# Kernel optimization log

Hardware: AMD Instinct MI355X
Metric: run time of the kernel (lower is better)

The kernel has to match this reference:

```python
import jax, jax.numpy as jnp
import numpy as np

D_EMBED = 1024


def setup_inputs() -> dict:
    key = jax.random.key(0)
    ks = jax.random.split(key, 8)
    B, S, D = 8, 2048, D_EMBED
    scale = 1.0 / np.sqrt(D)
    return {
        "embeddings": jax.random.normal(ks[0], (B, S, D), dtype=jnp.float32),
        "mask": jnp.zeros((B, S, S), dtype=jnp.float32),
        "Wq": jax.random.normal(ks[1], (D, D), dtype=jnp.float32) * scale,
        "bq": jax.random.normal(ks[2], (D,), dtype=jnp.float32) * 0.02,
        "Wk": jax.random.normal(ks[3], (D, D), dtype=jnp.float32) * scale,
        "bk": jax.random.normal(ks[4], (D,), dtype=jnp.float32) * 0.02,
        "Wv": jax.random.normal(ks[5], (D, D), dtype=jnp.float32) * scale,
        "bv": jax.random.normal(ks[6], (D,), dtype=jnp.float32) * 0.02,
    }


def reference(embeddings, mask, Wq, bq, Wk, bk, Wv, bv):
    # torch Linear: y = x @ W.T + b
    q = jnp.einsum('bsd,ed->bse', embeddings, Wq) + bq
    k = jnp.einsum('bsd,ed->bse', embeddings, Wk) + bk
    v = jnp.einsum('bsd,ed->bse', embeddings, Wv) + bv
    scores = jnp.einsum('bqd,bkd->bqk', q, k)
    # NOTE: faithful to source — mask added BEFORE scaling by 1/sqrt(d)
    scores = (scores + mask) * (1.0 / jnp.sqrt(jnp.float32(q.shape[-1])))
    attn = jax.nn.softmax(scores, axis=-1)
    return jnp.einsum('bqk,bkd->bqd', attn, v)
```

## Files before the change

### kernel.cpp

```cpp
#include <hip/hip_runtime.h>


#define B_SZ 8
#define SEQ  2048
#define DIM  1024
#define MROWS (B_SZ * SEQ)

typedef unsigned short u16;
typedef short short8 __attribute__((ext_vector_type(8)));
typedef unsigned short u16x4 __attribute__((ext_vector_type(4)));
typedef float f32x4 __attribute__((ext_vector_type(4)));

__device__ __forceinline__ u16 f2bf(float x) {
  unsigned int u = __float_as_uint(x);
  return (u16)((u + 0x7fffu + ((u >> 16) & 1u)) >> 16);
}
__device__ __forceinline__ float bf2f(u16 h) {
  return __uint_as_float(((unsigned int)h) << 16);
}

__device__ __forceinline__ int xcd_swz(int x, int nwg) {
  return (x & 7) * (nwg >> 3) + (x >> 3);
}

__device__ __forceinline__ void gload_lds16(const u16* g, u16* l) {
  __builtin_amdgcn_global_load_lds(
      (__attribute__((address_space(1))) void*)(g),
      (__attribute__((address_space(3))) void*)(l), 16, 0, 0);
}

__device__ __forceinline__ f32x4 mfma_bf16(short8 a, short8 b, f32x4 c) {
  asm("v_mfma_f32_16x16x32_bf16 %0, %1, %2, %0" : "+v"(c) : "v"(a), "v"(b));
  return c;
}

__device__ __forceinline__ void gemm256_core(const u16* __restrict__ Ag,
                                             const u16* __restrict__ Bg,
                                             int NT, size_t lda, size_t ldb,
                                             u16* sm, f32x4 (&acc)[8][4]) {
  const int tid = threadIdx.x;
  const int lane = tid & 63;
  const int wid = tid >> 6;
  const int wm = wid >> 2;
  const int wn = wid & 3;
  const int wm8 = wm << 3;
  const int wn4 = wn << 2;

  u16* sA = sm;
  u16* sB = sm + 32768;

  const int bb = (lane << 4) ^ (((lane >> 5) & 1) << 5);
  const int rins = bb >> 6;
  const int cins = (bb & 63) >> 1;
  const int s0 = wid, s1 = 8 + wid, s2 = 16 + wid, s3 = 24 + wid;
  const size_t aoff0 = (size_t)((s0 >> 1) * 16 + rins) * lda + ((s0 & 1) * 32 + cins);
  const size_t aoff1 = (size_t)((s1 >> 1) * 16 + rins) * lda + ((s1 & 1) * 32 + cins);
  const size_t aoff2 = (size_t)((s2 >> 1) * 16 + rins) * lda + ((s2 & 1) * 32 + cins);
  const size_t aoff3 = (size_t)((s3 >> 1) * 16 + rins) * lda + ((s3 & 1) * 32 + cins);
  const size_t boff0 = (size_t)((s0 >> 1) * 16 + rins) * ldb + ((s0 & 1) * 32 + cins);
  const size_t boff1 = (size_t)((s1 >> 1) * 16 + rins) * ldb + ((s1 & 1) * 32 + cins);
  const size_t boff2 = (size_t)((s2 >> 1) * 16 + rins) * ldb + ((s2 & 1) * 32 + cins);
  const size_t boff3 = (size_t)((s3 >> 1) * 16 + rins) * ldb + ((s3 & 1) * 32 + cins);
  const int wid512 = wid << 9;

  const int lof = ((lane & 15) << 6) + ((lane >> 4) << 4);
  const int loe = (lof ^ (((lane >> 3) & 1) << 5)) >> 1;

#define ISSUE_A(j, nb, kt) \
  gload_lds16(Ag + aoff##j + (size_t)(kt) * 64, sA + (nb) * 16384 + (j) * 4096 + wid512)
#define ISSUE_B(j, nb, kt) \
  gload_lds16(Bg + boff##j + (size_t)(kt) * 64, sB + (nb) * 16384 + (j) * 4096 + wid512)

  ISSUE_B(0, 0, 0); ISSUE_B(1, 0, 0); ISSUE_B(2, 0, 0); ISSUE_B(3, 0, 0);
  ISSUE_A(0, 0, 0); ISSUE_A(1, 0, 0); ISSUE_A(2, 0, 0); ISSUE_A(3, 0, 0);

  int buf = 0;
  for (int kt = 0; kt < NT; ++kt) {
    const int nk = kt + 1;
    const bool pre = nk < NT;
    const int nb = buf ^ 1;
    asm volatile("s_waitcnt vmcnt(1)" ::: "memory");
    __builtin_amdgcn_s_barrier();
    asm volatile("" ::: "memory");
    const u16* bufA = sA + buf * 16384;
    const u16* bufB = sB + buf * 16384;
    short8 bf[4][2];
#pragma unroll
    for (int n = 0; n < 4; ++n) {
      bf[n][0] = *(const short8*)(bufB + (wn4 + n) * 1024 + loe);
      bf[n][1] = *(const short8*)(bufB + (wn4 + n) * 1024 + 512 + loe);
    }
    {
      short8 af[2][2];
#pragma unroll
      for (int m = 0; m < 2; ++m) {
        af[m][0] = *(const short8*)(bufA + (wm8 + m) * 1024 + loe);
        af[m][1] = *(const short8*)(bufA + (wm8 + m) * 1024 + 512 + loe);
      }
      if (pre) { ISSUE_B(0, nb, nk); ISSUE_B(1, nb, nk); }
      __builtin_amdgcn_s_setprio(1);
#pragma unroll
      for (int m = 0; m < 2; ++m)
#pragma unroll
        for (int n = 0; n < 4; ++n) {
          acc[m][n] = mfma_bf16(af[m][0], bf[n][0], acc[m][n]);
          acc[m][n] = mfma_bf16(af[m][1], bf[n][1], acc[m][n]);
        }
      __builtin_amdgcn_s_setprio(0);
    }
    {
      short8 af[2][2];
#pragma unroll
      for (int m = 0; m < 2; ++m) {
        af[m][0] = *(const short8*)(bufA + (wm8 + 2 + m) * 1024 + loe);
        af[m][1] = *(const short8*)(bufA + (wm8 + 2 + m) * 1024 + 512 + loe);
      }
      if (pre) { ISSUE_B(2, nb, nk); ISSUE_B(3, nb, nk); }
      __builtin_amdgcn_s_setprio(1);
#pragma unroll
      for (int m = 0; m < 2; ++m)
#pragma unroll
        for (int n = 0; n < 4; ++n) {
          acc[2 + m][n] = mfma_bf16(af[m][0], bf[n][0], acc[2 + m][n]);
          acc[2 + m][n] = mfma_bf16(af[m][1], bf[n][1], acc[2 + m][n]);
        }
      __builtin_amdgcn_s_setprio(0);
    }
    if (pre) {
      asm volatile("s_waitcnt vmcnt(4)" ::: "memory");
    } else {
      asm volatile("s_waitcnt vmcnt(0)" ::: "memory");
    }
    __builtin_amdgcn_s_barrier();
    asm volatile("" ::: "memory");
    {
      short8 af[2][2];
#pragma unroll
      for (int m = 0; m < 2; ++m) {
        af[m][0] = *(const short8*)(bufA + (wm8 + 4 + m) * 1024 + loe);
        af[m][1] = *(const short8*)(bufA + (wm8 + 4 + m) * 1024 + 512 + loe);
      }
      if (pre) { ISSUE_A(0, nb, nk); ISSUE_A(1, nb, nk); }
      __builtin_amdgcn_s_setprio(1);
#pragma unroll
      for (int m = 0; m < 2; ++m)
#pragma unroll
        for (int n = 0; n < 4; ++n) {
          acc[4 + m][n] = mfma_bf16(af[m][0], bf[n][0], acc[4 + m][n]);
          acc[4 + m][n] = mfma_bf16(af[m][1], bf[n][1], acc[4 + m][n]);
        }
      __builtin_amdgcn_s_setprio(0);
    }
    {
      short8 af[2][2];
#pragma unroll
      for (int m = 0; m < 2; ++m) {
        af[m][0] = *(const short8*)(bufA + (wm8 + 6 + m) * 1024 + loe);
        af[m][1] = *(const short8*)(bufA + (wm8 + 6 + m) * 1024 + 512 + loe);
      }
      if (pre) { ISSUE_A(2, nb, nk); ISSUE_A(3, nb, nk); }
      __builtin_amdgcn_s_setprio(1);
#pragma unroll
      for (int m = 0; m < 2; ++m)
#pragma unroll
        for (int n = 0; n < 4; ++n) {
          acc[6 + m][n] = mfma_bf16(af[m][0], bf[n][0], acc[6 + m][n]);
          acc[6 + m][n] = mfma_bf16(af[m][1], bf[n][1], acc[6 + m][n]);
        }
      __builtin_amdgcn_s_setprio(0);
    }
    buf ^= 1;
  }
  asm volatile("s_nop 7\n\ts_nop 7\n\ts_nop 7" ::);
#undef ISSUE_A
#undef ISSUE_B
}

__global__ __launch_bounds__(256) void cvt_kernel(const float* __restrict__ in,
                                                  u16* __restrict__ out, int n4) {
  int i = blockIdx.x * 256 + threadIdx.x;
  if (i >= n4) return;
  float4 v = ((const float4*)in)[i];
  u16x4 o;
  o[0] = f2bf(v.x); o[1] = f2bf(v.y); o[2] = f2bf(v.z); o[3] = f2bf(v.w);
  ((u16x4*)out)[i] = o;
}

__global__ __launch_bounds__(512) void proj256_kernel(const u16* __restrict__ emb16,
                                                      const u16* __restrict__ Bq,
                                                      const u16* __restrict__ Bk,
                                                      const u16* __restrict__ Bv,
                                                      const float* __restrict__ bq,
                                                      const float* __restrict__ bk,
                                                      const float* __restrict__ bv,
                                                      u16* __restrict__ q16,
                                                      u16* __restrict__ k16,
                                                      u16* __restrict__ vT) {
  __shared__ __align__(16) u16 sm[65536];
  const int wg = xcd_swz(blockIdx.x, 768);
  const int lane = threadIdx.x & 63, wid = threadIdx.x >> 6;
  f32x4 acc[8][4] = {};
  if (wg < 512) {
    const int m0 = (wg >> 3) * 256;
    const int z = (wg >> 2) & 1;
    const int n0 = (wg & 3) * 256;
    gemm256_core(emb16 + (size_t)m0 * 1024, (z ? Bk : Bq) + (size_t)n0 * 1024,
                 16, 1024, 1024, sm, acc);
    const int rb = m0 + ((wid >> 2) << 7) + ((lane >> 4) << 2);
    const int cb = n0 + ((wid & 3) << 6) + (lane & 15);
    const float* bias = z ? bk : bq;
    u16* dst = z ? k16 : q16;
#pragma unroll
    for (int m = 0; m < 8; ++m)
#pragma unroll
      for (int n = 0; n < 4; ++n)
#pragma unroll
        for (int j = 0; j < 4; ++j) {
          int row = rb + m * 16 + j;
          int col = cb + n * 16;
          dst[(size_t)row * DIM + col] = f2bf(acc[m][n][j] + bias[col]);
        }
  } else {
    const int r = wg - 512;
    const int m0 = (r & 3) * 256;
    const int n0 = (r >> 2) * 256;
    gemm256_core(Bv + (size_t)m0 * 1024, emb16 + (size_t)n0 * 1024,
                 16, 1024, 1024, sm, acc);
    const int rb = m0 + ((wid >> 2) << 7) + ((lane >> 4) << 2);
    const int cb = n0 + ((wid & 3) << 6) + (lane & 15);
#pragma unroll
    for (int m = 0; m < 8; ++m)
#pragma unroll
      for (int n = 0; n < 4; ++n)
#pragma unroll
        for (int j = 0; j < 4; ++j) {
          int d = rb + m * 16 + j;
          int kg = cb + n * 16;
          int bi = kg >> 11, s = kg & 2047;
          vT[((size_t)bi << 21) + ((size_t)d << 11) + s] = f2bf(acc[m][n][j] + bv[d]);
        }
  }
}

__global__ __launch_bounds__(512) void scores256_kernel(const u16* __restrict__ q16,
                                                        const u16* __restrict__ k16,
                                                        const float* __restrict__ mask,
                                                        float* __restrict__ scF) {
  __shared__ __align__(16) u16 sm[65536];
  const int wg = xcd_swz(blockIdx.x, 512);
  const int b = wg >> 6;
  const int m0 = ((wg >> 3) & 7) * 256;
  const int n0 = (wg & 7) * 256;
  f32x4 acc[8][4] = {};
  gemm256_core(q16 + ((size_t)b * SEQ + m0) * DIM, k16 + ((size_t)b * SEQ + n0) * DIM,
               16, DIM, DIM, sm, acc);
  const int lane = threadIdx.x & 63, wid = threadIdx.x >> 6;
  const int rb = m0 + ((wid >> 2) << 7) + ((lane >> 4) << 2);
  const int cb = n0 + ((wid & 3) << 6) + (lane & 15);
#pragma unroll
  for (int m = 0; m < 8; ++m)
#pragma unroll
    for (int n = 0; n < 4; ++n)
#pragma unroll
      for (int j = 0; j < 4; ++j) {
        size_t idx = ((size_t)b * SEQ + rb + m * 16 + j) * SEQ + (cb + n * 16);
        scF[idx] = (acc[m][n][j] + mask[idx]) * 0.03125f;
      }
}

__global__ __launch_bounds__(512) void pv256_kernel(const u16* __restrict__ pr,
                                                    const u16* __restrict__ vt,
                                                    float* __restrict__ out) {
  __shared__ __align__(16) u16 sm[65536];
  const int wg = xcd_swz(blockIdx.x, 256);
  const int b = wg >> 5;
  const int m0 = ((wg >> 2) & 7) * 256;
  const int n0 = (wg & 3) * 256;
  f32x4 acc[8][4] = {};
  gemm256_core(pr + ((size_t)b * SEQ + m0) * (2 * SEQ), vt + ((size_t)b * DIM + n0) * SEQ,
               32, 2 * SEQ, SEQ, sm, acc);
  const int lane = threadIdx.x & 63, wid = threadIdx.x >> 6;
  const int rb = m0 + ((wid >> 2) << 7) + ((lane >> 4) << 2);
  const int cb = n0 + ((wid & 3) << 6) + (lane & 15);
#pragma unroll
  for (int m = 0; m < 8; ++m)
#pragma unroll
    for (int n = 0; n < 4; ++n)
#pragma unroll
      for (int j = 0; j < 4; ++j)
        out[((size_t)b * SEQ + rb + m * 16 + j) * DIM + (cb + n * 16)] = acc[m][n][j];
}

__global__ __launch_bounds__(256) void softmax_kernel(float* __restrict__ scF) {
  __shared__ float red[8];
  const size_t row = blockIdx.x;
  float* rowp = scF + row * SEQ;
  const int tid = threadIdx.x;
  float4 v0 = ((const float4*)rowp)[2 * tid];
  float4 v1 = ((const float4*)rowp)[2 * tid + 1];
  float f[8] = {v0.x, v0.y, v0.z, v0.w, v1.x, v1.y, v1.z, v1.w};
  float mx = f[0];
#pragma unroll
  for (int j = 1; j < 8; ++j) mx = fmaxf(mx, f[j]);
#pragma unroll
  for (int off = 1; off < 64; off <<= 1) mx = fmaxf(mx, __shfl_xor(mx, off));
  const int wid = tid >> 6, lane = tid & 63;
  if (lane == 0) red[wid] = mx;
  __syncthreads();
  mx = fmaxf(fmaxf(red[0], red[1]), fmaxf(red[2], red[3]));
  float e[8];
  float s = 0.f;
#pragma unroll
  for (int j = 0; j < 8; ++j) {
    e[j] = __expf(f[j] - mx);
    s += e[j];
  }
#pragma unroll
  for (int off = 1; off < 64; off <<= 1) s += __shfl_xor(s, off);
  if (lane == 0) red[4 + wid] = s;
  __syncthreads();
  s = (red[4] + red[5]) + (red[6] + red[7]);
  const float inv = 1.f / s;
  short8 o;
#pragma unroll
  for (int j = 0; j < 8; ++j) o[j] = (short)f2bf(e[j] * inv);
  *(short8*)((u16*)rowp + tid * 8) = o;
}

extern "C" void kernel_launch(void* const* d_in, const int* in_sizes, int n_in,
                              void* d_out, int out_size, void* d_ws, size_t ws_size,
                              hipStream_t stream) {
  const float* emb  = (const float*)d_in[0];
  const float* mask = (const float*)d_in[1];
  const float* Wq   = (const float*)d_in[2];
  const float* bq   = (const float*)d_in[3];
  const float* Wk   = (const float*)d_in[4];
  const float* bk   = (const float*)d_in[5];
  const float* Wv   = (const float*)d_in[6];
  const float* bv   = (const float*)d_in[7];
  float* out = (float*)d_out;

  const size_t M1 = 1024 * 1024;
  float* scF  = (float*)d_ws;
  u16* emb16 = (u16*)d_ws + 64 * M1;
  u16* Bq  = emb16 + 16 * M1;
  u16* Bk  = Bq + 1 * M1;
  u16* Bv  = Bk + 1 * M1;
  u16* q16 = Bv + 1 * M1;
  u16* k16 = q16 + 16 * M1;
  u16* vT  = k16 + 16 * M1;

  cvt_kernel<<<16384, 256, 0, stream>>>(emb, emb16, (int)(4 * M1));
  cvt_kernel<<<1024, 256, 0, stream>>>(Wq, Bq, (int)(M1 / 4));
  cvt_kernel<<<1024, 256, 0, stream>>>(Wk, Bk, (int)(M1 / 4));
  cvt_kernel<<<1024, 256, 0, stream>>>(Wv, Bv, (int)(M1 / 4));

  proj256_kernel<<<768, 512, 0, stream>>>(emb16, Bq, Bk, Bv, bq, bk, bv, q16, k16, vT);

  scores256_kernel<<<512, 512, 0, stream>>>(q16, k16, mask, scF);
  softmax_kernel<<<MROWS, 256, 0, stream>>>(scF);
  pv256_kernel<<<256, 512, 0, stream>>>((const u16*)scF, vT, out);
}
```

Measured before the change: 326.0 us.

## Switch to fp16 MFMA and store scores as fp16, moving mask add to softmax

All GEMM operands and intermediates go from bf16 to fp16 with v_mfma_f32_16x16x32_f16. The score matrix is now written as fp16 instead of fp32, which halves the traffic of writing, reading and rewriting the 8x2048x2048 scores. The mask read moves from the scores epilogue into the softmax kernel. fp16 has a narrower range than bf16, so there is some overflow risk, and scores are rounded to fp16 before softmax.

```diff
diff --git a/kernel.cpp b/kernel.cpp
--- a/kernel.cpp
+++ b/kernel.cpp
@@ -11,12 +11,12 @@
 typedef unsigned short u16x4 __attribute__((ext_vector_type(4)));
 typedef float f32x4 __attribute__((ext_vector_type(4)));
 
-__device__ __forceinline__ u16 f2bf(float x) {
-  unsigned int u = __float_as_uint(x);
-  return (u16)((u + 0x7fffu + ((u >> 16) & 1u)) >> 16);
-}
-__device__ __forceinline__ float bf2f(u16 h) {
-  return __uint_as_float(((unsigned int)h) << 16);
+__device__ __forceinline__ u16 f2h(float x) {
+  _Float16 h = (_Float16)x;
+  union { _Float16 f; u16 u; } c; c.f = h; return c.u;
+}
+__device__ __forceinline__ float h2f(u16 u) {
+  union { _Float16 f; u16 u; } c; c.u = u; return (float)c.f;
 }
 
 __device__ __forceinline__ int xcd_swz(int x, int nwg) {
@@ -29,8 +29,8 @@
       (__attribute__((address_space(3))) void*)(l), 16, 0, 0);
 }
 
-__device__ __forceinline__ f32x4 mfma_bf16(short8 a, short8 b, f32x4 c) {
-  asm("v_mfma_f32_16x16x32_bf16 %0, %1, %2, %0" : "+v"(c) : "v"(a), "v"(b));
+__device__ __forceinline__ f32x4 mfma_f16(short8 a, short8 b, f32x4 c) {
+  asm("v_mfma_f32_16x16x32_f16 %0, %1, %2, %0" : "+v"(c) : "v"(a), "v"(b));
   return c;
 }
 
@@ -103,8 +103,8 @@
       for (int m = 0; m < 2; ++m)
 #pragma unroll
         for (int n = 0; n < 4; ++n) {
-          acc[m][n] = mfma_bf16(af[m][0], bf[n][0], acc[m][n]);
-          acc[m][n] = mfma_bf16(af[m][1], bf[n][1], acc[m][n]);
+          acc[m][n] = mfma_f16(af[m][0], bf[n][0], acc[m][n]);
+          acc[m][n] = mfma_f16(af[m][1], bf[n][1], acc[m][n]);
         }
       __builtin_amdgcn_s_setprio(0);
     }
@@ -121,8 +121,8 @@
       for (int m = 0; m < 2; ++m)
 #pragma unroll
         for (int n = 0; n < 4; ++n) {
-          acc[2 + m][n] = mfma_bf16(af[m][0], bf[n][0], acc[2 + m][n]);
-          acc[2 + m][n] = mfma_bf16(af[m][1], bf[n][1], acc[2 + m][n]);
+          acc[2 + m][n] = mfma_f16(af[m][0], bf[n][0], acc[2 + m][n]);
+          acc[2 + m][n] = mfma_f16(af[m][1], bf[n][1], acc[2 + m][n]);
         }
       __builtin_amdgcn_s_setprio(0);
     }
@@ -146,8 +146,8 @@
       for (int m = 0; m < 2; ++m)
 #pragma unroll
         for (int n = 0; n < 4; ++n) {
-          acc[4 + m][n] = mfma_bf16(af[m][0], bf[n][0], acc[4 + m][n]);
-          acc[4 + m][n] = mfma_bf16(af[m][1], bf[n][1], acc[4 + m][n]);
+          acc[4 + m][n] = mfma_f16(af[m][0], bf[n][0], acc[4 + m][n]);
+          acc[4 + m][n] = mfma_f16(af[m][1], bf[n][1], acc[4 + m][n]);
         }
       __builtin_amdgcn_s_setprio(0);
     }
@@ -164,8 +164,8 @@
       for (int m = 0; m < 2; ++m)
 #pragma unroll
         for (int n = 0; n < 4; ++n) {
-          acc[6 + m][n] = mfma_bf16(af[m][0], bf[n][0], acc[6 + m][n]);
-          acc[6 + m][n] = mfma_bf16(af[m][1], bf[n][1], acc[6 + m][n]);
+          acc[6 + m][n] = mfma_f16(af[m][0], bf[n][0], acc[6 + m][n]);
+          acc[6 + m][n] = mfma_f16(af[m][1], bf[n][1], acc[6 + m][n]);
         }
       __builtin_amdgcn_s_setprio(0);
     }
@@ -182,7 +182,7 @@
   if (i >= n4) return;
   float4 v = ((const float4*)in)[i];
   u16x4 o;
-  o[0] = f2bf(v.x); o[1] = f2bf(v.y); o[2] = f2bf(v.z); o[3] = f2bf(v.w);
+  o[0] = f2h(v.x); o[1] = f2h(v.y); o[2] = f2h(v.z); o[3] = f2h(v.w);
   ((u16x4*)out)[i] = o;
 }
 
@@ -218,7 +218,7 @@
         for (int j = 0; j < 4; ++j) {
           int row = rb + m * 16 + j;
           int col = cb + n * 16;
-          dst[(size_t)row * DIM + col] = f2bf(acc[m][n][j] + bias[col]);
+          dst[(size_t)row * DIM + col] = f2h(acc[m][n][j] + bias[col]);
         }
   } else {
     const int r = wg - 512;
@@ -237,15 +237,14 @@
           int d = rb + m * 16 + j;
           int kg = cb + n * 16;
           int bi = kg >> 11, s = kg & 2047;
-          vT[((size_t)bi << 21) + ((size_t)d << 11) + s] = f2bf(acc[m][n][j] + bv[d]);
+          vT[((size_t)bi << 21) + ((size_t)d << 11) + s] = f2h(acc[m][n][j] + bv[d]);
         }
   }
 }
 
 __global__ __launch_bounds__(512) void scores256_kernel(const u16* __restrict__ q16,
                                                         const u16* __restrict__ k16,
-                                                        const float* __restrict__ mask,
-                                                        float* __restrict__ scF) {
+                                                        u16* __restrict__ scH) {
   __shared__ __align__(16) u16 sm[65536];
   const int wg = xcd_swz(blockIdx.x, 512);
   const int b = wg >> 6;
@@ -264,8 +263,50 @@
 #pragma unroll
       for (int j = 0; j < 4; ++j) {
         size_t idx = ((size_t)b * SEQ + rb + m * 16 + j) * SEQ + (cb + n * 16);
-        scF[idx] = (acc[m][n][j] + mask[idx]) * 0.03125f;
-      }
+        scH[idx] = f2h(acc[m][n][j] * 0.03125f);
+      }
+}
+
+__global__ __launch_bounds__(256) void softmax_kernel(u16* __restrict__ scH,
+                                                      const float* __restrict__ mask) {
+  __shared__ float red[8];
+  const size_t row = blockIdx.x;
+  u16* rowp = scH + row * SEQ;
+  const float* mrow = mask + row * SEQ;
+  const int tid = threadIdx.x;
+  short8 raw = *(const short8*)(rowp + tid * 8);
+  float4 m0 = ((const float4*)mrow)[2 * tid];
+  float4 m1 = ((const float4*)mrow)[2 * tid + 1];
+  float mk[8] = {m0.x, m0.y, m0.z, m0.w, m1.x, m1.y, m1.z, m1.w};
+  float f[8];
+#pragma unroll
+  for (int j = 0; j < 8; ++j) f[j] = h2f((u16)raw[j]) + mk[j] * 0.03125f;
+  float mx = f[0];
+#pragma unroll
+  for (int j = 1; j < 8; ++j) mx = fmaxf(mx, f[j]);
+#pragma unroll
+  for (int off = 1; off < 64; off <<= 1) mx = fmaxf(mx, __shfl_xor(mx, off));
+  const int wid = tid >> 6, lane = tid & 63;
+  if (lane == 0) red[wid] = mx;
+  __syncthreads();
+  mx = fmaxf(fmaxf(red[0], red[1]), fmaxf(red[2], red[3]));
+  float e[8];
+  float s = 0.f;
+#pragma unroll
+  for (int j = 0; j < 8; ++j) {
+    e[j] = __expf(f[j] - mx);
+    s += e[j];
+  }
+#pragma unroll
+  for (int off = 1; off < 64; off <<= 1) s += __shfl_xor(s, off);
+  if (lane == 0) red[4 + wid] = s;
+  __syncthreads();
+  s = (red[4] + red[5]) + (red[6] + red[7]);
+  const float inv = 1.f / s;
+  short8 o;
+#pragma unroll
+  for (int j = 0; j < 8; ++j) o[j] = (short)f2h(e[j] * inv);
+  *(short8*)(rowp + tid * 8) = o;
 }
 
 __global__ __launch_bounds__(512) void pv256_kernel(const u16* __restrict__ pr,
@@ -277,8 +318,8 @@
   const int m0 = ((wg >> 2) & 7) * 256;
   const int n0 = (wg & 3) * 256;
   f32x4 acc[8][4] = {};
-  gemm256_core(pr + ((size_t)b * SEQ + m0) * (2 * SEQ), vt + ((size_t)b * DIM + n0) * SEQ,
-               32, 2 * SEQ, SEQ, sm, acc);
+  gemm256_core(pr + ((size_t)b * SEQ + m0) * SEQ, vt + ((size_t)b * DIM + n0) * SEQ,
+               32, SEQ, SEQ, sm, acc);
   const int lane = threadIdx.x & 63, wid = threadIdx.x >> 6;
   const int rb = m0 + ((wid >> 2) << 7) + ((lane >> 4) << 2);
   const int cb = n0 + ((wid & 3) << 6) + (lane & 15);
@@ -289,42 +330,6 @@
 #pragma unroll
       for (int j = 0; j < 4; ++j)
         out[((size_t)b * SEQ + rb + m * 16 + j) * DIM + (cb + n * 16)] = acc[m][n][j];
-}
-
-__global__ __launch_bounds__(256) void softmax_kernel(float* __restrict__ scF) {
-  __shared__ float red[8];
-  const size_t row = blockIdx.x;
-  float* rowp = scF + row * SEQ;
-  const int tid = threadIdx.x;
-  float4 v0 = ((const float4*)rowp)[2 * tid];
-  float4 v1 = ((const float4*)rowp)[2 * tid + 1];
-  float f[8] = {v0.x, v0.y, v0.z, v0.w, v1.x, v1.y, v1.z, v1.w};
-  float mx = f[0];
-#pragma unroll
-  for (int j = 1; j < 8; ++j) mx = fmaxf(mx, f[j]);
-#pragma unroll
-  for (int off = 1; off < 64; off <<= 1) mx = fmaxf(mx, __shfl_xor(mx, off));
-  const int wid = tid >> 6, lane = tid & 63;
-  if (lane == 0) red[wid] = mx;
-  __syncthreads();
-  mx = fmaxf(fmaxf(red[0], red[1]), fmaxf(red[2], red[3]));
-  float e[8];
-  float s = 0.f;
-#pragma unroll
-  for (int j = 0; j < 8; ++j) {
-    e[j] = __expf(f[j] - mx);
-    s += e[j];
-  }
-#pragma unroll
-  for (int off = 1; off < 64; off <<= 1) s += __shfl_xor(s, off);
-  if (lane == 0) red[4 + wid] = s;
-  __syncthreads();
-  s = (red[4] + red[5]) + (red[6] + red[7]);
-  const float inv = 1.f / s;
-  short8 o;
-#pragma unroll
-  for (int j = 0; j < 8; ++j) o[j] = (short)f2bf(e[j] * inv);
-  *(short8*)((u16*)rowp + tid * 8) = o;
 }
 
 extern "C" void kernel_launch(void* const* d_in, const int* in_sizes, int n_in,
@@ -341,8 +346,8 @@
   float* out = (float*)d_out;
 
   const size_t M1 = 1024 * 1024;
-  float* scF  = (float*)d_ws;
-  u16* emb16 = (u16*)d_ws + 64 * M1;
+  u16* scH   = (u16*)d_ws;
+  u16* emb16 = scH + 32 * M1;
   u16* Bq  = emb16 + 16 * M1;
   u16* Bk  = Bq + 1 * M1;
   u16* Bv  = Bk + 1 * M1;
@@ -357,7 +362,7 @@
 
   proj256_kernel<<<768, 512, 0, stream>>>(emb16, Bq, Bk, Bv, bq, bk, bv, q16, k16, vT);
 
-  scores256_kernel<<<512, 512, 0, stream>>>(q16, k16, mask, scF);
-  softmax_kernel<<<MROWS, 256, 0, stream>>>(scF);
-  pv256_kernel<<<256, 512, 0, stream>>>((const u16*)scF, vT, out);
-}
+  scores256_kernel<<<512, 512, 0, stream>>>(q16, k16, scH);
+  softmax_kernel<<<MROWS, 256, 0, stream>>>(scH, mask);
+  pv256_kernel<<<256, 512, 0, stream>>>((const u16*)scH, vT, out);
+}
```

Result: faster. 305.8 us (-6.2%).
